# Kernel optimization log

Hardware: AMD Instinct MI355X
Metric: run time of the kernel (lower is better)

## Reference

```python
import jax, jax.numpy as jnp
import numpy as np


def setup_inputs() -> dict:
    key = jax.random.key(0)
    k1, k2, k3, k4, k5 = jax.random.split(key, 5)
    B, T, D, H = 32, 512, 1024, 1024
    s = 1.0 / np.sqrt(H)
    return {
        "inputs": jax.random.normal(k1, (B, T, D), dtype=jnp.float32),
        "Wx": jax.random.normal(k2, (4 * H, D), dtype=jnp.float32) * s,
        "bx": jax.random.normal(k3, (4 * H,), dtype=jnp.float32) * s,
        "Wh": jax.random.normal(k4, (4 * H, H), dtype=jnp.float32) * s,
        "bh": jax.random.normal(k5, (4 * H,), dtype=jnp.float32) * s,
    }


def reference(inputs, Wx, bx, Wh, bh):
    # inputs: [B, T, D]; Wx: [4H, D]; Wh: [4H, H]
    B, T, D = inputs.shape
    H = Wh.shape[1]
    # Input-to-hidden projection for all timesteps at once: [B, T, 4H]
    xg = jnp.einsum('btd,gd->btg', inputs, Wx) + bx

    def step(carry, x_t):
        h, c = carry  # [B, H] each
        gates = x_t + h @ Wh.T + bh  # [B, 4H]
        i, f, g, o = jnp.split(gates, 4, axis=-1)
        i = jax.nn.sigmoid(i)
        f = jax.nn.sigmoid(f)
        g = jax.nn.sigmoid(g)  # original code uses sigmoid for cell gate
        o = jax.nn.sigmoid(o)
        c = c * f + i * g
        h = o * jnp.tanh(c)
        return (h, c), h

    h0 = jnp.zeros((B, H), dtype=inputs.dtype)
    c0 = jnp.zeros((B, H), dtype=inputs.dtype)
    _, hs = jax.lax.scan(step, (h0, c0), jnp.transpose(xg, (1, 0, 2)))  # hs: [T, B, H]
    return jnp.transpose(hs, (1, 0, 2))  # [B, T, H]
```

## Files before the change

kernel.cpp:

```cpp
#include <hip/hip_runtime.h>
#include <hip/hip_bf16.h>
#include <math.h>

#define B_ 32
#define T_ 512
#define D_ 1024
#define H_ 1024
#define G4 4096
#define BT 16384
#define NWG 64

using bf16x8 = __attribute__((ext_vector_type(8))) short;
using f32x4  = __attribute__((ext_vector_type(4))) float;
typedef unsigned long long u64;

__device__ __forceinline__ float sigm(float x) { return 1.0f / (1.0f + __expf(-x)); }

#define OFF_FLG   0ull
#define OFF_HBUF  4096ull
#define OFF_WHB   (OFF_HBUF + 131072ull)
#define OFF_WXB   (OFF_WHB + 8388608ull)
#define OFF_INPB  (OFF_WXB + 8388608ull)
#define OFF_BXH   (OFF_INPB + 33554432ull)
#define OFF_XG    (OFF_BXH + 16384ull)
#define WS_NEEDED (OFF_XG + 134217728ull)

#define SMEM_GBUF   65536
#define SMEM_LFLAG  74240
#define SMEM_TOTAL  74304

__global__ __launch_bounds__(256) void convert_all(
    const float* __restrict__ inp, const float* __restrict__ Wx,
    const float* __restrict__ bx, const float* __restrict__ Wh,
    const float* __restrict__ bh,
    __hip_bfloat16* __restrict__ inp_b, __hip_bfloat16* __restrict__ Wx_b,
    __hip_bfloat16* __restrict__ Wh_b, float* __restrict__ bxh)
{
    const int gid = blockIdx.x * 256 + threadIdx.x;
    {
        const float4* s = (const float4*)inp + (size_t)gid * 4;
        #pragma unroll
        for (int v = 0; v < 4; ++v) {
            float4 f = s[v];
            size_t base = (size_t)gid * 16 + v * 4;
            inp_b[base + 0] = __float2bfloat16(f.x);
            inp_b[base + 1] = __float2bfloat16(f.y);
            inp_b[base + 2] = __float2bfloat16(f.z);
            inp_b[base + 3] = __float2bfloat16(f.w);
        }
    }
    {
        float4 fx = ((const float4*)Wx)[gid];
        float4 fh = ((const float4*)Wh)[gid];
        size_t base = (size_t)gid * 4;
        Wx_b[base + 0] = __float2bfloat16(fx.x);
        Wx_b[base + 1] = __float2bfloat16(fx.y);
        Wx_b[base + 2] = __float2bfloat16(fx.z);
        Wx_b[base + 3] = __float2bfloat16(fx.w);
        Wh_b[base + 0] = __float2bfloat16(fh.x);
        Wh_b[base + 1] = __float2bfloat16(fh.y);
        Wh_b[base + 2] = __float2bfloat16(fh.z);
        Wh_b[base + 3] = __float2bfloat16(fh.w);
    }
    if (gid < G4) bxh[gid] = bx[gid] + bh[gid];
}

__global__ __launch_bounds__(256) void xg_gemm(
    const __hip_bfloat16* __restrict__ X,
    const __hip_bfloat16* __restrict__ Wxb,
    const float* __restrict__ bxh,
    __hip_bfloat16* __restrict__ xg)
{
    __shared__ __align__(16) char As[16384];
    __shared__ __align__(16) char Bs[16384];

    const int m0 = blockIdx.x * 128;
    const int n0 = blockIdx.y * 128;
    const int tid = threadIdx.x;
    const int lane = tid & 63;
    const int wv = tid >> 6;
    const int vr = wv >> 1, vc = wv & 1;
    const int l15 = lane & 15;
    const int kg = (lane >> 4) * 8;

    const int srow_ = wv * 32 + (lane >> 3);
    const int scolb = (lane & 7) * 16;

    f32x4 acc[4][4] = {};

    for (int k0 = 0; k0 < D_; k0 += 64) {
        #pragma unroll
        for (int c = 0; c < 4; ++c) {
            const int row = srow_ + c * 8;
            const int cb  = scolb ^ ((row & 7) << 4);
            const char* ga = (const char*)X   + (size_t)(m0 + row) * 2048 + k0 * 2 + cb;
            const char* gb = (const char*)Wxb + (size_t)(n0 + row) * 2048 + k0 * 2 + cb;
            __builtin_amdgcn_global_load_lds(
                (const __attribute__((address_space(1))) void*)ga,
                (__attribute__((address_space(3))) void*)(As + wv * 4096 + c * 1024),
                16, 0, 0);
            __builtin_amdgcn_global_load_lds(
                (const __attribute__((address_space(1))) void*)gb,
                (__attribute__((address_space(3))) void*)(Bs + wv * 4096 + c * 1024),
                16, 0, 0);
        }
        __syncthreads();

        #pragma unroll
        for (int kk = 0; kk < 64; kk += 32) {
            bf16x8 af[4], bf[4];
            #pragma unroll
            for (int mi = 0; mi < 4; ++mi) {
                const int row = vr * 64 + mi * 16 + l15;
                af[mi] = *(const bf16x8*)(As + row * 128 + (((kk + kg) * 2) ^ ((row & 7) << 4)));
            }
            #pragma unroll
            for (int ni = 0; ni < 4; ++ni) {
                const int col = vc * 64 + ni * 16 + l15;
                bf[ni] = *(const bf16x8*)(Bs + col * 128 + (((kk + kg) * 2) ^ ((col & 7) << 4)));
            }
            #pragma unroll
            for (int mi = 0; mi < 4; ++mi)
                #pragma unroll
                for (int ni = 0; ni < 4; ++ni)
                    acc[mi][ni] = __builtin_amdgcn_mfma_f32_16x16x32_bf16(
                        af[mi], bf[ni], acc[mi][ni], 0, 0, 0);
        }
        __syncthreads();
    }

    #pragma unroll
    for (int ni = 0; ni < 4; ++ni) {
        const int col = n0 + vc * 64 + ni * 16 + l15;
        const int qq = col >> 10, ww = (col >> 4) & 63, jj = col & 15;
        const float bias = bxh[col];
        #pragma unroll
        for (int mi = 0; mi < 4; ++mi) {
            const int r0 = m0 + vr * 64 + mi * 16 + ((lane >> 4) << 2);
            #pragma unroll
            for (int r = 0; r < 4; ++r) {
                const int row = r0 + r;
                const int bb = row >> 9, tt = row & 511;
                xg[(((size_t)tt * NWG + ww) * 4 + qq) * 512 + bb * 16 + jj] =
                    __float2bfloat16(acc[mi][ni][r] + bias);
            }
        }
    }
}

__global__ __launch_bounds__(512, 2) void lstm_scan(
    const __hip_bfloat16* __restrict__ xg,
    const __hip_bfloat16* __restrict__ Whb,
    __hip_bfloat16* __restrict__ hseq,
    unsigned int* __restrict__ flags)
{
    extern __shared__ char smem[];
    float* gbuf = (float*)(smem + SMEM_GBUF);
    int* lds_flag = (int*)(smem + SMEM_LFLAG);

    const int w    = blockIdx.x;
    const int tid  = threadIdx.x;
    const int lane = tid & 63;
    const int wave = tid >> 6;
    const int mwave = wave >> 2;
    const int q     = wave & 3;
    const int l15   = lane & 15;
    const int kg    = (lane >> 4) * 8;

    if (tid == 0) *lds_flag = 0;

    bf16x8 bfrag[32];
    {
        const char* wrow = (const char*)(Whb + (size_t)(q * 1024 + w * 16 + l15) * H_);
        #pragma unroll
        for (int i = 0; i < 32; ++i) {
            u64 lo = __hip_atomic_load((const u64*)(wrow + (i * 32 + kg) * 2),
                                       __ATOMIC_RELAXED, __HIP_MEMORY_SCOPE_AGENT);
            u64 hi = __hip_atomic_load((const u64*)(wrow + (i * 32 + kg) * 2 + 8),
                                       __ATOMIC_RELAXED, __HIP_MEMORY_SCOPE_AGENT);
            union { u64 qv[2]; bf16x8 v; } u;
            u.qv[0] = lo; u.qv[1] = hi;
            bfrag[i] = u.v;
        }
    }

    const int pb  = tid >> 4;
    const int pjj = tid & 15;
    float cst = 0.0f;

    const int dbr   = mwave * 16 + ((lane >> 4) << 2);
    const int arow  = mwave * 16 + l15;
    const int abase = arow * 2048;
    const int axor  = (arow & 7) << 4;
    const int srow  = wave * 4 + (lane >> 4);
    const int ql    = lane & 15;

    for (int t = 0; t < T_; ++t) {
        float xgv[4];
        {
            const size_t sbase = (((size_t)t * NWG + w) * 4 + q) * 512;
            #pragma unroll
            for (int r = 0; r < 4; ++r)
                xgv[r] = __bfloat162float(xg[sbase + (dbr + r) * 16 + l15]);
        }

        f32x4 acc = {};
        if (t > 0) {
            if (wave == 0) {
                const unsigned int* fp = flags + lane * 16;
                while (__hip_atomic_load(fp, __ATOMIC_RELAXED, __HIP_MEMORY_SCOPE_AGENT)
                       < (unsigned)t)
                    __builtin_amdgcn_s_sleep(1);
                __hip_atomic_store(lds_flag, t, __ATOMIC_RELAXED,
                                   __HIP_MEMORY_SCOPE_WORKGROUP);
            } else {
                while (__hip_atomic_load(lds_flag, __ATOMIC_RELAXED,
                                         __HIP_MEMORY_SCOPE_WORKGROUP) < t)
                    __builtin_amdgcn_s_sleep(1);
            }
            asm volatile("" ::: "memory");

            {
                const bf16x8* src = (const bf16x8*)(hseq + ((size_t)(t - 1) * B_ + srow) * H_);
                #pragma unroll
                for (int j = 0; j < 8; ++j) {
                    bf16x8 v = src[ql + j * 16];
                    *(bf16x8*)(smem + srow * 2048 + (((ql + j * 16) * 16) ^ ((srow & 7) << 4))) = v;
                }
            }
            __syncthreads();

            f32x4 a0 = {}, a1 = {}, a2 = {}, a3 = {};
            #pragma unroll
            for (int i = 0; i < 8; ++i) {
                bf16x8 v0 = *(const bf16x8*)(smem + abase + ((((4 * i + 0) * 64) + kg * 2) ^ axor));
                bf16x8 v1 = *(const bf16x8*)(smem + abase + ((((4 * i + 1) * 64) + kg * 2) ^ axor));
                bf16x8 v2 = *(const bf16x8*)(smem + abase + ((((4 * i + 2) * 64) + kg * 2) ^ axor));
                bf16x8 v3 = *(const bf16x8*)(smem + abase + ((((4 * i + 3) * 64) + kg * 2) ^ axor));
                a0 = __builtin_amdgcn_mfma_f32_16x16x32_bf16(v0, bfrag[4 * i + 0], a0, 0, 0, 0);
                a1 = __builtin_amdgcn_mfma_f32_16x16x32_bf16(v1, bfrag[4 * i + 1], a1, 0, 0, 0);
                a2 = __builtin_amdgcn_mfma_f32_16x16x32_bf16(v2, bfrag[4 * i + 2], a2, 0, 0, 0);
                a3 = __builtin_amdgcn_mfma_f32_16x16x32_bf16(v3, bfrag[4 * i + 3], a3, 0, 0, 0);
            }
            acc = (a0 + a1) + (a2 + a3);
        }

        #pragma unroll
        for (int r = 0; r < 4; ++r)
            gbuf[((dbr + r) * 4 + q) * 17 + l15] = acc[r] + xgv[r];
        __syncthreads();

        {
            float gi = sigm(gbuf[(pb * 4 + 0) * 17 + pjj]);
            float gf = sigm(gbuf[(pb * 4 + 1) * 17 + pjj]);
            float gg = sigm(gbuf[(pb * 4 + 2) * 17 + pjj]);
            float go = sigm(gbuf[(pb * 4 + 3) * 17 + pjj]);
            cst = cst * gf + gi * gg;
            float h = go * tanhf(cst);
            __hip_bfloat16 hb = __float2bfloat16(h);
            unsigned short hs_;
            __builtin_memcpy(&hs_, &hb, 2);
            unsigned hu = hs_;
            unsigned h1 = __shfl_down(hu, 1, 64);
            unsigned h2 = __shfl_down(hu, 2, 64);
            unsigned h3 = __shfl_down(hu, 3, 64);
            if ((lane & 3) == 0) {
                u64 pv = (u64)hu | ((u64)h1 << 16) | ((u64)h2 << 32) | ((u64)h3 << 48);
                u64* dst = (u64*)(hseq + ((size_t)t * B_ + pb) * H_ + w * 16 + pjj);
                __hip_atomic_store(dst, pv, __ATOMIC_RELAXED, __HIP_MEMORY_SCOPE_AGENT);
            }
        }
        __syncthreads();

        if (t < T_ - 1 && tid == 0)
            __hip_atomic_store(flags + w * 16, (unsigned)(t + 1),
                               __ATOMIC_RELAXED, __HIP_MEMORY_SCOPE_AGENT);
    }
}

__global__ __launch_bounds__(256) void expand_out(
    const __hip_bfloat16* __restrict__ hseq, float* __restrict__ out)
{
    const size_t gid = (size_t)blockIdx.x * 256 + threadIdx.x;
    const size_t lin = gid * 8;
    const int t = (int)(lin >> 15);
    const int b = (int)((lin >> 10) & 31);
    const int h = (int)(lin & 1023);
    bf16x8 v = *(const bf16x8*)(hseq + lin);
    float* o = out + ((size_t)b * T_ + t) * H_ + h;
    #pragma unroll
    for (int i = 0; i < 8; ++i) {
        unsigned short s = (unsigned short)v[i];
        __hip_bfloat16 bv;
        __builtin_memcpy(&bv, &s, 2);
        o[i] = __bfloat162float(bv);
    }
}

__global__ __launch_bounds__(256) void lstm_step(
    const float* __restrict__ inp, const float* __restrict__ Wx,
    const float* __restrict__ bx, const float* __restrict__ Wh,
    const float* __restrict__ bh, float* __restrict__ out,
    float* __restrict__ c_state, int t)
{
    const int tid = threadIdx.x;
    const int lane = tid & 63;
    const int khalf = lane & 1;
    const int b = lane >> 1;
    const int j = blockIdx.x * 4 + (tid >> 6);
    const int k0 = khalf * (D_ / 2);
    float a0 = 0.f, a1 = 0.f, a2 = 0.f, a3 = 0.f;
    {
        const float* xrow = inp + ((size_t)b * T_ + t) * D_ + k0;
        const float* w0 = Wx + (size_t)(0 * H_ + j) * D_ + k0;
        const float* w1 = Wx + (size_t)(1 * H_ + j) * D_ + k0;
        const float* w2 = Wx + (size_t)(2 * H_ + j) * D_ + k0;
        const float* w3 = Wx + (size_t)(3 * H_ + j) * D_ + k0;
        for (int kk = 0; kk < D_ / 2; kk += 4) {
            float4 xv = *(const float4*)(xrow + kk);
            float4 v0 = *(const float4*)(w0 + kk), v1 = *(const float4*)(w1 + kk);
            float4 v2 = *(const float4*)(w2 + kk), v3 = *(const float4*)(w3 + kk);
            a0 = fmaf(xv.x, v0.x, fmaf(xv.y, v0.y, fmaf(xv.z, v0.z, fmaf(xv.w, v0.w, a0))));
            a1 = fmaf(xv.x, v1.x, fmaf(xv.y, v1.y, fmaf(xv.z, v1.z, fmaf(xv.w, v1.w, a1))));
            a2 = fmaf(xv.x, v2.x, fmaf(xv.y, v2.y, fmaf(xv.z, v2.z, fmaf(xv.w, v2.w, a2))));
            a3 = fmaf(xv.x, v3.x, fmaf(xv.y, v3.y, fmaf(xv.z, v3.z, fmaf(xv.w, v3.w, a3))));
        }
    }
    if (t > 0) {
        const float* hrow = out + ((size_t)b * T_ + (t - 1)) * H_ + k0;
        const float* w0 = Wh + (size_t)(0 * H_ + j) * H_ + k0;
        const float* w1 = Wh + (size_t)(1 * H_ + j) * H_ + k0;
        const float* w2 = Wh + (size_t)(2 * H_ + j) * H_ + k0;
        const float* w3 = Wh + (size_t)(3 * H_ + j) * H_ + k0;
        for (int kk = 0; kk < H_ / 2; kk += 4) {
            float4 hv = *(const float4*)(hrow + kk);
            float4 v0 = *(const float4*)(w0 + kk), v1 = *(const float4*)(w1 + kk);
            float4 v2 = *(const float4*)(w2 + kk), v3 = *(const float4*)(w3 + kk);
            a0 = fmaf(hv.x, v0.x, fmaf(hv.y, v0.y, fmaf(hv.z, v0.z, fmaf(hv.w, v0.w, a0))));
            a1 = fmaf(hv.x, v1.x, fmaf(hv.y, v1.y, fmaf(hv.z, v1.z, fmaf(hv.w, v1.w, a1))));
            a2 = fmaf(hv.x, v2.x, fmaf(hv.y, v2.y, fmaf(hv.z, v2.z, fmaf(hv.w, v2.w, a2))));
            a3 = fmaf(hv.x, v3.x, fmaf(hv.y, v3.y, fmaf(hv.z, v3.z, fmaf(hv.w, v3.w, a3))));
        }
    }
    a0 += __shfl_xor(a0, 1, 64); a1 += __shfl_xor(a1, 1, 64);
    a2 += __shfl_xor(a2, 1, 64); a3 += __shfl_xor(a3, 1, 64);
    if (khalf == 0) {
        float gi = sigm(a0 + bx[0 * H_ + j] + bh[0 * H_ + j]);
        float gf = sigm(a1 + bx[1 * H_ + j] + bh[1 * H_ + j]);
        float gg = sigm(a2 + bx[2 * H_ + j] + bh[2 * H_ + j]);
        float go = sigm(a3 + bx[3 * H_ + j] + bh[3 * H_ + j]);
        size_t ci = (size_t)b * H_ + j;
        float c = (t > 0) ? c_state[ci] : 0.0f;
        c = c * gf + gi * gg;
        c_state[ci] = c;
        out[((size_t)b * T_ + t) * H_ + j] = go * tanhf(c);
    }
}

extern "C" void kernel_launch(void* const* d_in, const int* in_sizes, int n_in,
                              void* d_out, int out_size, void* d_ws, size_t ws_size,
                              hipStream_t stream) {
    const float* inp = (const float*)d_in[0];
    const float* Wx  = (const float*)d_in[1];
    const float* bx  = (const float*)d_in[2];
    const float* Wh  = (const float*)d_in[3];
    const float* bh  = (const float*)d_in[4];
    float* out = (float*)d_out;
    char* ws = (char*)d_ws;

    if (ws_size < WS_NEEDED) {
        float* c_state = (float*)d_ws;
        for (int t = 0; t < T_; ++t)
            lstm_step<<<dim3(H_ / 4), dim3(256), 0, stream>>>(inp, Wx, bx, Wh, bh, out, c_state, t);
        return;
    }

    unsigned int*    flags = (unsigned int*)(ws + OFF_FLG);
    __hip_bfloat16*  Whb   = (__hip_bfloat16*)(ws + OFF_WHB);
    __hip_bfloat16*  Wxb   = (__hip_bfloat16*)(ws + OFF_WXB);
    __hip_bfloat16*  inp_b = (__hip_bfloat16*)(ws + OFF_INPB);
    float*           bxh   = (float*)(ws + OFF_BXH);
    __hip_bfloat16*  xg    = (__hip_bfloat16*)(ws + OFF_XG);
    __hip_bfloat16*  hseq  = inp_b;

    hipMemsetAsync(flags, 0, 4096, stream);

    convert_all<<<dim3(4096), dim3(256), 0, stream>>>(inp, Wx, bx, Wh, bh, inp_b, Wxb, Whb, bxh);

    xg_gemm<<<dim3(BT / 128, G4 / 128), dim3(256), 0, stream>>>(inp_b, Wxb, bxh, xg);

    static bool attr_set = false;
    if (!attr_set) {
        hipFuncSetAttribute((const void*)lstm_scan,
                            hipFuncAttributeMaxDynamicSharedMemorySize, SMEM_TOTAL);
        attr_set = true;
    }
    lstm_scan<<<dim3(NWG), dim3(512), SMEM_TOTAL, stream>>>(xg, Whb, hseq, flags);

    expand_out<<<dim3((BT * H_ / 8) / 256), dim3(256), 0, stream>>>(hseq, out);
}
```

Before: 1.943 ms.

## Replace flag-based cross-block sync with sequence-tagged double-buffered hidden state

```diff
diff --git a/kernel.cpp b/kernel.cpp
--- a/kernel.cpp
+++ b/kernel.cpp
@@ -13,12 +13,12 @@
 using bf16x8 = __attribute__((ext_vector_type(8))) short;
 using f32x4  = __attribute__((ext_vector_type(4))) float;
 typedef unsigned long long u64;
+typedef unsigned int u32;
 
 __device__ __forceinline__ float sigm(float x) { return 1.0f / (1.0f + __expf(-x)); }
 
-#define OFF_FLG   0ull
-#define OFF_HBUF  4096ull
-#define OFF_WHB   (OFF_HBUF + 131072ull)
+#define OFF_TB    0ull
+#define OFF_WHB   262144ull
 #define OFF_WXB   (OFF_WHB + 8388608ull)
 #define OFF_INPB  (OFF_WXB + 8388608ull)
 #define OFF_BXH   (OFF_INPB + 33554432ull)
@@ -26,8 +26,7 @@
 #define WS_NEEDED (OFF_XG + 134217728ull)
 
 #define SMEM_GBUF   65536
-#define SMEM_LFLAG  74240
-#define SMEM_TOTAL  74304
+#define SMEM_TOTAL  74240
 
 __global__ __launch_bounds__(256) void convert_all(
     const float* __restrict__ inp, const float* __restrict__ Wx,
@@ -148,15 +147,14 @@
     }
 }
 
-__global__ __launch_bounds__(512, 2) void lstm_scan(
+__global__ __launch_bounds__(512) void lstm_scan(
     const __hip_bfloat16* __restrict__ xg,
     const __hip_bfloat16* __restrict__ Whb,
-    __hip_bfloat16* __restrict__ hseq,
-    unsigned int* __restrict__ flags)
+    float* __restrict__ out,
+    u64* __restrict__ tb)
 {
     extern __shared__ char smem[];
     float* gbuf = (float*)(smem + SMEM_GBUF);
-    int* lds_flag = (int*)(smem + SMEM_LFLAG);
 
     const int w    = blockIdx.x;
     const int tid  = threadIdx.x;
@@ -167,8 +165,6 @@
     const int l15   = lane & 15;
     const int kg    = (lane >> 4) * 8;
 
-    if (tid == 0) *lds_flag = 0;
-
     bf16x8 bfrag[32];
     {
         const char* wrow = (const char*)(Whb + (size_t)(q * 1024 + w * 16 + l15) * H_);
@@ -186,6 +182,7 @@
 
     const int pb  = tid >> 4;
     const int pjj = tid & 15;
+    const int jcol = w * 16 + pjj;
     float cst = 0.0f;
 
     const int dbr   = mwave * 16 + ((lane >> 4) << 2);
@@ -206,26 +203,29 @@
 
         f32x4 acc = {};
         if (t > 0) {
-            if (wave == 0) {
-                const unsigned int* fp = flags + lane * 16;
-                while (__hip_atomic_load(fp, __ATOMIC_RELAXED, __HIP_MEMORY_SCOPE_AGENT)
-                       < (unsigned)t)
-                    __builtin_amdgcn_s_sleep(1);
-                __hip_atomic_store(lds_flag, t, __ATOMIC_RELAXED,
-                                   __HIP_MEMORY_SCOPE_WORKGROUP);
-            } else {
-                while (__hip_atomic_load(lds_flag, __ATOMIC_RELAXED,
-                                         __HIP_MEMORY_SCOPE_WORKGROUP) < t)
-                    __builtin_amdgcn_s_sleep(1);
-            }
-            asm volatile("" ::: "memory");
-
-            {
-                const bf16x8* src = (const bf16x8*)(hseq + ((size_t)(t - 1) * B_ + srow) * H_);
+            const u64* src = tb + ((size_t)((t - 1) & 1) * B_ + srow) * 512 + ql * 32;
+            const u32 expect = (u32)(t - 1);
+            #pragma unroll
+            for (int half = 0; half < 2; ++half) {
+                u64 g[16];
                 #pragma unroll
-                for (int j = 0; j < 8; ++j) {
-                    bf16x8 v = src[ql + j * 16];
-                    *(bf16x8*)(smem + srow * 2048 + (((ql + j * 16) * 16) ^ ((srow & 7) << 4))) = v;
+                for (int j = 0; j < 16; ++j)
+                    g[j] = __hip_atomic_load(src + half * 16 + j,
+                                             __ATOMIC_RELAXED, __HIP_MEMORY_SCOPE_AGENT);
+                #pragma unroll
+                for (int j = 0; j < 16; ++j)
+                    while ((u32)g[j] != expect)
+                        g[j] = __hip_atomic_load(src + half * 16 + j,
+                                                 __ATOMIC_RELAXED, __HIP_MEMORY_SCOPE_AGENT);
+                #pragma unroll
+                for (int c = 0; c < 4; ++c) {
+                    uint4 pk;
+                    pk.x = (u32)(g[c * 4 + 0] >> 32);
+                    pk.y = (u32)(g[c * 4 + 1] >> 32);
+                    pk.z = (u32)(g[c * 4 + 2] >> 32);
+                    pk.w = (u32)(g[c * 4 + 3] >> 32);
+                    const int byteoff = ql * 128 + half * 64 + c * 16;
+                    *(uint4*)(smem + srow * 2048 + (byteoff ^ ((srow & 7) << 4))) = pk;
                 }
             }
             __syncthreads();
@@ -256,44 +256,21 @@
             float gg = sigm(gbuf[(pb * 4 + 2) * 17 + pjj]);
             float go = sigm(gbuf[(pb * 4 + 3) * 17 + pjj]);
             cst = cst * gf + gi * gg;
-            float h = go * tanhf(cst);
+            float e2 = __expf(2.0f * cst);
+            float h = go * (1.0f - 2.0f / (e2 + 1.0f));
+
             __hip_bfloat16 hb = __float2bfloat16(h);
             unsigned short hs_;
             __builtin_memcpy(&hs_, &hb, 2);
-            unsigned hu = hs_;
-            unsigned h1 = __shfl_down(hu, 1, 64);
-            unsigned h2 = __shfl_down(hu, 2, 64);
-            unsigned h3 = __shfl_down(hu, 3, 64);
-            if ((lane & 3) == 0) {
-                u64 pv = (u64)hu | ((u64)h1 << 16) | ((u64)h2 << 32) | ((u64)h3 << 48);
-                u64* dst = (u64*)(hseq + ((size_t)t * B_ + pb) * H_ + w * 16 + pjj);
-                __hip_atomic_store(dst, pv, __ATOMIC_RELAXED, __HIP_MEMORY_SCOPE_AGENT);
-            }
-        }
-        __syncthreads();
-
-        if (t < T_ - 1 && tid == 0)
-            __hip_atomic_store(flags + w * 16, (unsigned)(t + 1),
-                               __ATOMIC_RELAXED, __HIP_MEMORY_SCOPE_AGENT);
-    }
-}
-
-__global__ __launch_bounds__(256) void expand_out(
-    const __hip_bfloat16* __restrict__ hseq, float* __restrict__ out)
-{
-    const size_t gid = (size_t)blockIdx.x * 256 + threadIdx.x;
-    const size_t lin = gid * 8;
-    const int t = (int)(lin >> 15);
-    const int b = (int)((lin >> 10) & 31);
-    const int h = (int)(lin & 1023);
-    bf16x8 v = *(const bf16x8*)(hseq + lin);
-    float* o = out + ((size_t)b * T_ + t) * H_ + h;
-    #pragma unroll
-    for (int i = 0; i < 8; ++i) {
-        unsigned short s = (unsigned short)v[i];
-        __hip_bfloat16 bv;
-        __builtin_memcpy(&bv, &s, 2);
-        o[i] = __bfloat162float(bv);
+            u32 hu = hs_;
+            u32 hup = __shfl_down(hu, 1, 64);
+            if (!(pjj & 1)) {
+                u64 val = ((u64)(hu | (hup << 16)) << 32) | (u64)(u32)t;
+                __hip_atomic_store(tb + ((size_t)(t & 1) * B_ + pb) * 512 + w * 8 + (pjj >> 1),
+                                   val, __ATOMIC_RELAXED, __HIP_MEMORY_SCOPE_AGENT);
+            }
+            out[((size_t)pb * T_ + t) * H_ + jcol] = h;
+        }
     }
 }
 
@@ -375,15 +352,14 @@
         return;
     }
 
-    unsigned int*    flags = (unsigned int*)(ws + OFF_FLG);
+    u64*             tb    = (u64*)(ws + OFF_TB);
     __hip_bfloat16*  Whb   = (__hip_bfloat16*)(ws + OFF_WHB);
     __hip_bfloat16*  Wxb   = (__hip_bfloat16*)(ws + OFF_WXB);
     __hip_bfloat16*  inp_b = (__hip_bfloat16*)(ws + OFF_INPB);
     float*           bxh   = (float*)(ws + OFF_BXH);
     __hip_bfloat16*  xg    = (__hip_bfloat16*)(ws + OFF_XG);
-    __hip_bfloat16*  hseq  = inp_b;
-
-    hipMemsetAsync(flags, 0, 4096, stream);
+
+    hipMemsetAsync(tb, 0xFF, 262144, stream);
 
     convert_all<<<dim3(4096), dim3(256), 0, stream>>>(inp, Wx, bx, Wh, bh, inp_b, Wxb, Whb, bxh);
 
@@ -395,7 +371,5 @@
                             hipFuncAttributeMaxDynamicSharedMemorySize, SMEM_TOTAL);
         attr_set = true;
     }
-    lstm_scan<<<dim3(NWG), dim3(512), SMEM_TOTAL, stream>>>(xg, Whb, hseq, flags);
-
-    expand_out<<<dim3((BT * H_ / 8) / 256), dim3(256), 0, stream>>>(hseq, out);
-}
+    lstm_scan<<<dim3(NWG), dim3(512), SMEM_TOTAL, stream>>>(xg, Whb, out, tb);
+}
```

Result: slower. 7.272 ms (+274.2%).
